# Optimization experiments

Hardware: AMD Instinct MI355X
Metric: run time of the kernel (lower is better)

Reference implementation:

```python
import jax, jax.numpy as jnp
import numpy as np

NUM_HEADS = 16
D_MODEL = 1024
DEPTH = D_MODEL // NUM_HEADS
B, S = 4, 1024  # q,k seq len = S; v seq len = S-1


def setup_inputs() -> dict:
    key = jax.random.key(0)
    ks = jax.random.split(key, 6)
    scale = 1.0 / np.sqrt(D_MODEL)
    return {
        "v": jax.random.normal(ks[0], (B, S - 1, D_MODEL), dtype=jnp.float32),
        "k": jax.random.normal(ks[1], (B, S, D_MODEL), dtype=jnp.float32),
        "q": jax.random.normal(ks[2], (B, S, D_MODEL), dtype=jnp.float32),
        "mask": jnp.zeros((B, S - 1, S - 1), dtype=jnp.float32),
        "Wv": jax.random.normal(ks[3], (D_MODEL, D_MODEL), dtype=jnp.float32) * scale,
        "bv": jnp.zeros((D_MODEL,), dtype=jnp.float32),
        "Wd": jax.random.normal(ks[4], (D_MODEL, D_MODEL), dtype=jnp.float32) * scale,
        "bd": jnp.zeros((D_MODEL,), dtype=jnp.float32),
    }


def _split_heads(x):
    # (B, T, d_model) -> (B, H, T, depth)
    b, t, _ = x.shape
    return x.reshape(b, t, NUM_HEADS, DEPTH).transpose(0, 2, 1, 3)


def reference(v, k, q, mask, Wv, bv, Wd, bd):
    # 3-D q/k path: qq=q, kk=k (q_layers/k_layers/wq/wk unused)
    vv = v @ Wv + bv                       # (B, S-1, d_model)
    qh = _split_heads(q)                   # (B, H, S, depth)
    kh = _split_heads(k)                   # (B, H, S, depth)
    vh = _split_heads(vv)                  # (B, H, S-1, depth)

    scores = jnp.einsum('bhqd,bhkd->bhqk', qh, kh)      # (B, H, S, S)
    scores = scores[:, :, 1:, :-1]                      # (B, H, S-1, S-1)
    dk = jnp.asarray(DEPTH, scores.dtype)
    nl = jax.nn.relu(scores / jnp.sqrt(dk))
    nl = nl + mask[:, None, :, :] * (-1e9)
    att = jax.nn.softmax(nl, axis=-1)                   # (B, H, S-1, S-1)

    out = jnp.einsum('bhqk,bhkd->bhqd', att, vh)        # (B, H, S-1, depth)
    out = out.transpose(0, 2, 1, 3).reshape(v.shape[0], -1, D_MODEL)  # (B, S-1, d_model)
    output = out @ Wd + bd
    return output, att
```

## Files before the change

### kernel.cpp

```cpp
#include <hip/hip_runtime.h>
#include <hip/hip_bf16.h>

#define NUM_HEADS 16
#define DM 1024
#define DEPTH 64
#define BB 4
#define SS 1024
#define SL 1023
#define M_ROWS (BB*SL)

typedef __attribute__((ext_vector_type(8))) short short8;
typedef __attribute__((ext_vector_type(4))) float floatx4;

__device__ inline unsigned short f2bf(float f) {
  __hip_bfloat16 hb = __float2bfloat16(f);
  return *reinterpret_cast<unsigned short*>(&hb);
}
__device__ inline short8 ld_frag(const unsigned short* p) {
  return *reinterpret_cast<const short8*>(p);
}

#define GLDS(g, l) __builtin_amdgcn_global_load_lds( \
    (const __attribute__((address_space(1))) void*)(g), \
    (__attribute__((address_space(3))) void*)(l), 16, 0, 0)

__global__ __launch_bounds__(256) void f32_to_bf16_vec(
    const float* __restrict__ in, unsigned short* __restrict__ out, int n8)
{
  int i = blockIdx.x * 256 + threadIdx.x;
  if (i >= n8) return;
  const float4 f0 = ((const float4*)in)[(size_t)i * 2];
  const float4 f1 = ((const float4*)in)[(size_t)i * 2 + 1];
  unsigned short t[8];
  t[0]=f2bf(f0.x); t[1]=f2bf(f0.y); t[2]=f2bf(f0.z); t[3]=f2bf(f0.w);
  t[4]=f2bf(f1.x); t[5]=f2bf(f1.y); t[6]=f2bf(f1.z); t[7]=f2bf(f1.w);
  ((uint4*)out)[i] = *(uint4*)t;
}

__global__ __launch_bounds__(256) void transpose_to_bf16(
    const float* __restrict__ W, unsigned short* __restrict__ WT)
{
  __shared__ unsigned short tile[64][72];
  const int tid = threadIdx.x;
  const int k0 = blockIdx.y * 64, n0 = blockIdx.x * 64;
  {
    const int kl = tid >> 2, nc = (tid & 3) * 16;
    const float* src = W + (size_t)(k0 + kl) * DM + n0 + nc;
    #pragma unroll
    for (int j = 0; j < 16; j += 4) {
      float4 f = *(const float4*)(src + j);
      tile[nc + j + 0][kl] = f2bf(f.x);
      tile[nc + j + 1][kl] = f2bf(f.y);
      tile[nc + j + 2][kl] = f2bf(f.z);
      tile[nc + j + 3][kl] = f2bf(f.w);
    }
  }
  __syncthreads();
  {
    const int nl = tid >> 2, kc = (tid & 3) * 16;
    unsigned short tmp[16];
    #pragma unroll
    for (int j = 0; j < 16; j++) tmp[j] = tile[nl][kc + j];
    unsigned short* dst = WT + (size_t)(n0 + nl) * DM + k0 + kc;
    *(uint4*)&dst[0] = *(uint4*)&tmp[0];
    *(uint4*)&dst[8] = *(uint4*)&tmp[8];
  }
}

template <bool OUT_BF16>
__global__ __launch_bounds__(256) void gemm_bt(
    const unsigned short* __restrict__ A,
    const unsigned short* __restrict__ BT,
    const float* __restrict__ bias,
    void* __restrict__ Cv, int M)
{
  constexpr int BM = 64, BN = 128, BK = 32;
  __shared__ __align__(16) unsigned short As[2][BM * BK];
  __shared__ __align__(16) unsigned short Bs[2][BN * BK];

  const int tid = threadIdx.x;
  const int w = tid >> 6, lane = tid & 63, q4 = lane >> 4, l16 = lane & 15;
  const int wm = w >> 1, wn = w & 1;
  const int rb = blockIdx.y * BM;
  const int cb = blockIdx.x * BN;

  const int a_row = tid >> 2;
  const int a_slot = (tid & 3) ^ ((a_row >> 1) & 3);
  int a_grow = rb + a_row; if (a_grow >= M) a_grow = M - 1;
  const unsigned short* a_src = A + (size_t)a_grow * DM + a_slot * 8;
  const int b_row0 = tid >> 2;
  const int b_row1 = 64 + (tid >> 2);
  const int b_slot0 = (tid & 3) ^ ((b_row0 >> 1) & 3);
  const int b_slot1 = (tid & 3) ^ ((b_row1 >> 1) & 3);
  const unsigned short* b_src0 = BT + (size_t)(cb + b_row0) * DM + b_slot0 * 8;
  const unsigned short* b_src1 = BT + (size_t)(cb + b_row1) * DM + b_slot1 * 8;

  int aoff[2], boff[4];
  #pragma unroll
  for (int i = 0; i < 2; i++) {
    int r = wm * 32 + i * 16 + l16;
    aoff[i] = r * BK + ((q4 ^ ((r >> 1) & 3)) * 8);
  }
  #pragma unroll
  for (int j = 0; j < 4; j++) {
    int r = wn * 64 + j * 16 + l16;
    boff[j] = r * BK + ((q4 ^ ((r >> 1) & 3)) * 8);
  }

  floatx4 acc[2][4];
  #pragma unroll
  for (int i = 0; i < 2; i++)
    #pragma unroll
    for (int j = 0; j < 4; j++) acc[i][j] = (floatx4){0.f,0.f,0.f,0.f};

  GLDS(a_src,  &As[0][tid * 8]);
  GLDS(b_src0, &Bs[0][tid * 8]);
  GLDS(b_src1, &Bs[0][2048 + tid * 8]);
  __syncthreads();

  int cur = 0;
  constexpr int NT = DM / BK;
  for (int t = 0; t < NT; ++t) {
    if (t + 1 < NT) {
      const int kn = (t + 1) * BK;
      GLDS(a_src + kn,  &As[cur ^ 1][tid * 8]);
      GLDS(b_src0 + kn, &Bs[cur ^ 1][tid * 8]);
      GLDS(b_src1 + kn, &Bs[cur ^ 1][2048 + tid * 8]);
    }
    short8 af[2], bfr[4];
    #pragma unroll
    for (int i = 0; i < 2; i++) af[i] = ld_frag(&As[cur][aoff[i]]);
    #pragma unroll
    for (int j = 0; j < 4; j++) bfr[j] = ld_frag(&Bs[cur][boff[j]]);
    #pragma unroll
    for (int i = 0; i < 2; i++)
      #pragma unroll
      for (int j = 0; j < 4; j++)
        acc[i][j] = __builtin_amdgcn_mfma_f32_16x16x32_bf16(af[i], bfr[j], acc[i][j], 0, 0, 0);
    __syncthreads();
    cur ^= 1;
  }

  #pragma unroll
  for (int j = 0; j < 4; j++) {
    int col = cb + wn * 64 + j * 16 + l16;
    float bb = bias[col];
    #pragma unroll
    for (int i = 0; i < 2; i++) {
      #pragma unroll
      for (int r = 0; r < 4; r++) {
        int m = rb + wm * 32 + i * 16 + q4 * 4 + r;
        if (m < M) {
          float val = acc[i][j][r] + bb;
          if (OUT_BF16) ((unsigned short*)Cv)[(size_t)m * DM + col] = f2bf(val);
          else          ((float*)Cv)[(size_t)m * DM + col] = val;
        }
      }
    }
  }
}

__global__ __launch_bounds__(256) void attn_kernel(
    const float* __restrict__ Q, const float* __restrict__ Kg,
    const float* __restrict__ Mask, const unsigned short* __restrict__ VV,
    float* __restrict__ Att, unsigned short* __restrict__ Out2)
{
  const int qt = blockIdx.x, h = blockIdx.y, b = blockIdx.z;
  const int tid = threadIdx.x;
  const int w = tid >> 6, lane = tid & 63, q4 = lane >> 4, l16 = lane & 15;
  const int qi0 = qt * 64;
  const int qb = w * 16;

  __shared__ unsigned short qsh[64][72];
  __shared__ unsigned short ksh[64][72];
  __shared__ unsigned short vshT[64][72];
  __shared__ unsigned short psh[4][16][72];

  {
    int qr = tid >> 2, d0 = (tid & 3) * 16;
    int qi = qi0 + qr;
    unsigned short tmp[16];
    if (qi < SL) {
      const float* src = Q + ((size_t)b * SS + qi + 1) * DM + h * DEPTH + d0;
      #pragma unroll
      for (int j = 0; j < 16; j += 4) {
        float4 f = *(const float4*)(src + j);
        tmp[j+0]=f2bf(f.x); tmp[j+1]=f2bf(f.y); tmp[j+2]=f2bf(f.z); tmp[j+3]=f2bf(f.w);
      }
    } else {
      #pragma unroll
      for (int j = 0; j < 16; j++) tmp[j] = 0;
    }
    *(uint4*)&qsh[qr][d0]     = *(uint4*)&tmp[0];
    *(uint4*)&qsh[qr][d0 + 8] = *(uint4*)&tmp[8];
  }

  auto stageK = [&](int kt) {
    int kr = tid >> 2, d0 = (tid & 3) * 16;
    int kj = kt * 64 + kr;
    unsigned short tmp[16];
    if (kj < SL) {
      const float* src = Kg + ((size_t)b * SS + kj) * DM + h * DEPTH + d0;
      #pragma unroll
      for (int j = 0; j < 16; j += 4) {
        float4 f = *(const float4*)(src + j);
        tmp[j+0]=f2bf(f.x); tmp[j+1]=f2bf(f.y); tmp[j+2]=f2bf(f.z); tmp[j+3]=f2bf(f.w);
      }
    } else {
      #pragma unroll
      for (int j = 0; j < 16; j++) tmp[j] = 0;
    }
    *(uint4*)&ksh[kr][d0]     = *(uint4*)&tmp[0];
    *(uint4*)&ksh[kr][d0 + 8] = *(uint4*)&tmp[8];
  };

  auto stageV = [&](int kt) {
    int d = tid & 63, k16 = (tid >> 6) * 16;
    unsigned short tmp[16];
    #pragma unroll
    for (int j = 0; j < 16; j++) {
      int kj = kt * 64 + k16 + j;
      tmp[j] = (kj < SL) ? VV[((size_t)b * SL + kj) * DM + h * DEPTH + d] : (unsigned short)0;
    }
    *(uint4*)&vshT[d][k16]     = *(uint4*)&tmp[0];
    *(uint4*)&vshT[d][k16 + 8] = *(uint4*)&tmp[8];
  };

  __syncthreads();

  float rsv[4] = {0.f, 0.f, 0.f, 0.f};
  for (int kt = 0; kt < 16; kt++) {
    __syncthreads();
    stageK(kt);
    __syncthreads();
    #pragma unroll
    for (int nt = 0; nt < 4; nt++) {
      floatx4 s = (floatx4){0.f,0.f,0.f,0.f};
      s = __builtin_amdgcn_mfma_f32_16x16x32_bf16(
            ld_frag(&qsh[qb + l16][q4*8]), ld_frag(&ksh[nt*16 + l16][q4*8]), s, 0,0,0);
      s = __builtin_amdgcn_mfma_f32_16x16x32_bf16(
            ld_frag(&qsh[qb + l16][32 + q4*8]), ld_frag(&ksh[nt*16 + l16][32 + q4*8]), s, 0,0,0);
      int kj = kt * 64 + nt * 16 + l16;
      bool kv = kj < SL;
      int qi_b = qi0 + qb + q4 * 4;
      const float* mp = Mask + ((size_t)b * SL + qi_b) * SL + kj;
      #pragma unroll
      for (int r = 0; r < 4; r++) {
        int qi = qi_b + r;
        float mval = (kv && qi < SL) ? mp[(size_t)r * SL] : 0.f;
        float sv = fmaxf(s[r] * 0.125f, 0.f) + mval * (-1e9f);
        float p = kv ? __expf(sv) : 0.f;
        rsv[r] += p;
      }
    }
  }
  #pragma unroll
  for (int r = 0; r < 4; r++) {
    #pragma unroll
    for (int off = 1; off < 16; off <<= 1) rsv[r] += __shfl_xor(rsv[r], off, 64);
  }
  float inv[4];
  #pragma unroll
  for (int r = 0; r < 4; r++) inv[r] = 1.f / rsv[r];

  floatx4 oacc[4];
  #pragma unroll
  for (int i = 0; i < 4; i++) oacc[i] = (floatx4){0.f,0.f,0.f,0.f};

  for (int kt = 0; kt < 16; kt++) {
    __syncthreads();
    stageK(kt);
    stageV(kt);
    __syncthreads();
    #pragma unroll
    for (int nt = 0; nt < 4; nt++) {
      floatx4 s = (floatx4){0.f,0.f,0.f,0.f};
      s = __builtin_amdgcn_mfma_f32_16x16x32_bf16(
            ld_frag(&qsh[qb + l16][q4*8]), ld_frag(&ksh[nt*16 + l16][q4*8]), s, 0,0,0);
      s = __builtin_amdgcn_mfma_f32_16x16x32_bf16(
            ld_frag(&qsh[qb + l16][32 + q4*8]), ld_frag(&ksh[nt*16 + l16][32 + q4*8]), s, 0,0,0);
      int kj = kt * 64 + nt * 16 + l16;
      bool kv = kj < SL;
      int qi_b = qi0 + qb + q4 * 4;
      const float* mp = Mask + ((size_t)b * SL + qi_b) * SL + kj;
      #pragma unroll
      for (int r = 0; r < 4; r++) {
        int qi = qi_b + r;
        bool qv = qi < SL;
        float mval = (kv && qv) ? mp[(size_t)r * SL] : 0.f;
        float sv = fmaxf(s[r] * 0.125f, 0.f) + mval * (-1e9f);
        float p = kv ? __expf(sv) : 0.f;
        float pn = p * inv[r];
        if (kv && qv)
          Att[(((size_t)(b * NUM_HEADS + h)) * SL + qi) * SL + kj] = pn;
        psh[w][q4 * 4 + r][nt * 16 + l16] = f2bf(pn);
      }
    }
    short8 pa0 = ld_frag(&psh[w][l16][q4 * 8]);
    short8 pa1 = ld_frag(&psh[w][l16][32 + q4 * 8]);
    #pragma unroll
    for (int nt2 = 0; nt2 < 4; nt2++) {
      oacc[nt2] = __builtin_amdgcn_mfma_f32_16x16x32_bf16(
                    pa0, ld_frag(&vshT[nt2*16 + l16][q4*8]), oacc[nt2], 0,0,0);
      oacc[nt2] = __builtin_amdgcn_mfma_f32_16x16x32_bf16(
                    pa1, ld_frag(&vshT[nt2*16 + l16][32 + q4*8]), oacc[nt2], 0,0,0);
    }
  }

  #pragma unroll
  for (int nt2 = 0; nt2 < 4; nt2++) {
    #pragma unroll
    for (int r = 0; r < 4; r++) {
      int qi = qi0 + qb + q4 * 4 + r;
      if (qi < SL)
        Out2[((size_t)b * SL + qi) * DM + h * DEPTH + nt2 * 16 + l16] = f2bf(oacc[nt2][r]);
    }
  }
}

extern "C" void kernel_launch(void* const* d_in, const int* in_sizes, int n_in,
                              void* d_out, int out_size, void* d_ws, size_t ws_size,
                              hipStream_t stream) {
  const float* v    = (const float*)d_in[0];
  const float* k    = (const float*)d_in[1];
  const float* q    = (const float*)d_in[2];
  const float* mask = (const float*)d_in[3];
  const float* Wv   = (const float*)d_in[4];
  const float* bv   = (const float*)d_in[5];
  const float* Wd   = (const float*)d_in[6];
  const float* bd   = (const float*)d_in[7];

  float* out = (float*)d_out;
  float* att = out + (size_t)M_ROWS * DM;
  unsigned short* vv   = (unsigned short*)d_ws;
  unsigned short* out2 = vv + (size_t)M_ROWS * DM;

  unsigned short* WvT = (unsigned short*)att;
  unsigned short* vbf = WvT + (size_t)DM * DM;
  unsigned short* WdT = vv;

  const int n8 = (M_ROWS * DM) / 8;

  f32_to_bf16_vec<<<dim3((n8 + 255) / 256), 256, 0, stream>>>(v, vbf, n8);
  transpose_to_bf16<<<dim3(16, 16), 256, 0, stream>>>(Wv, WvT);
  gemm_bt<true><<<dim3(DM/128, (M_ROWS+63)/64), 256, 0, stream>>>(vbf, WvT, bv, (void*)vv, M_ROWS);
  attn_kernel<<<dim3(16, NUM_HEADS, BB), 256, 0, stream>>>(q, k, mask, vv, att, out2);
  transpose_to_bf16<<<dim3(16, 16), 256, 0, stream>>>(Wd, WdT);
  gemm_bt<false><<<dim3(DM/128, (M_ROWS+63)/64), 256, 0, stream>>>(out2, WdT, bd, (void*)out, M_ROWS);
}
```

Before: 667.0 us.

## Triple-buffer GEMM with BK=64 and swap attention grid order

The bf16 GEMM now uses a K tile of 64 with a three-stage LDS ring, fed by direct global-to-LDS loads. It uses explicit vmcnt waits and barriers so two future tiles stay in flight while the current one runs through MFMA, with a new XOR swizzle over 8 groups. The fp32 output GEMM uses nontemporal stores. The attention grid is reordered so heads vary fastest, which changes L2 locality between neighbouring blocks. The larger LDS footprint may reduce occupancy, and the hand-written waitcnt counts must match the number of issued loads exactly.

```diff
diff --git a/kernel.cpp b/kernel.cpp
--- a/kernel.cpp
+++ b/kernel.cpp
@@ -19,6 +19,8 @@
 __device__ inline short8 ld_frag(const unsigned short* p) {
   return *reinterpret_cast<const short8*>(p);
 }
+
+#define SWZ(row, g) (((g) ^ ((row) & 7)))
 
 #define GLDS(g, l) __builtin_amdgcn_global_load_lds( \
     (const __attribute__((address_space(1))) void*)(g), \
@@ -74,9 +76,9 @@
     const float* __restrict__ bias,
     void* __restrict__ Cv, int M)
 {
-  constexpr int BM = 64, BN = 128, BK = 32;
-  __shared__ __align__(16) unsigned short As[2][BM * BK];
-  __shared__ __align__(16) unsigned short Bs[2][BN * BK];
+  constexpr int BM = 64, BN = 128, BK = 64;
+  __shared__ __align__(16) unsigned short As[3][BM * BK];
+  __shared__ __align__(16) unsigned short Bs[3][BN * BK];
 
   const int tid = threadIdx.x;
   const int w = tid >> 6, lane = tid & 63, q4 = lane >> 4, l16 = lane & 15;
@@ -84,28 +86,44 @@
   const int rb = blockIdx.y * BM;
   const int cb = blockIdx.x * BN;
 
-  const int a_row = tid >> 2;
-  const int a_slot = (tid & 3) ^ ((a_row >> 1) & 3);
-  int a_grow = rb + a_row; if (a_grow >= M) a_grow = M - 1;
-  const unsigned short* a_src = A + (size_t)a_grow * DM + a_slot * 8;
-  const int b_row0 = tid >> 2;
-  const int b_row1 = 64 + (tid >> 2);
-  const int b_slot0 = (tid & 3) ^ ((b_row0 >> 1) & 3);
-  const int b_slot1 = (tid & 3) ^ ((b_row1 >> 1) & 3);
-  const unsigned short* b_src0 = BT + (size_t)(cb + b_row0) * DM + b_slot0 * 8;
-  const unsigned short* b_src1 = BT + (size_t)(cb + b_row1) * DM + b_slot1 * 8;
-
-  int aoff[2], boff[4];
-  #pragma unroll
-  for (int i = 0; i < 2; i++) {
-    int r = wm * 32 + i * 16 + l16;
-    aoff[i] = r * BK + ((q4 ^ ((r >> 1) & 3)) * 8);
-  }
-  #pragma unroll
-  for (int j = 0; j < 4; j++) {
-    int r = wn * 64 + j * 16 + l16;
-    boff[j] = r * BK + ((q4 ^ ((r >> 1) & 3)) * 8);
-  }
+  const int wbase = __builtin_amdgcn_readfirstlane(w * 512);
+
+  const int srow = tid >> 3;
+  const int lg   = (tid & 7) ^ (srow & 7);
+  int ar0 = rb + srow;       if (ar0 >= M) ar0 = M - 1;
+  int ar1 = rb + 32 + srow;  if (ar1 >= M) ar1 = M - 1;
+  const unsigned short* a_src0 = A + (size_t)ar0 * DM + lg * 8;
+  const unsigned short* a_src1 = A + (size_t)ar1 * DM + lg * 8;
+  const unsigned short* b_src0 = BT + (size_t)(cb      + srow) * DM + lg * 8;
+  const unsigned short* b_src1 = BT + (size_t)(cb + 32 + srow) * DM + lg * 8;
+  const unsigned short* b_src2 = BT + (size_t)(cb + 64 + srow) * DM + lg * 8;
+  const unsigned short* b_src3 = BT + (size_t)(cb + 96 + srow) * DM + lg * 8;
+
+  auto stage = [&](int t, unsigned short* Ab, unsigned short* Bb) {
+    const int kn = t * BK;
+    GLDS(a_src0 + kn, Ab + wbase);
+    GLDS(a_src1 + kn, Ab + 2048 + wbase);
+    GLDS(b_src0 + kn, Bb + wbase);
+    GLDS(b_src1 + kn, Bb + 2048 + wbase);
+    GLDS(b_src2 + kn, Bb + 4096 + wbase);
+    GLDS(b_src3 + kn, Bb + 6144 + wbase);
+  };
+
+  int aoff[2][2], boff[4][2];
+  #pragma unroll
+  for (int i = 0; i < 2; i++)
+    #pragma unroll
+    for (int hf = 0; hf < 2; hf++) {
+      int r = wm * 32 + i * 16 + l16;
+      aoff[i][hf] = r * BK + SWZ(r, q4 + 4 * hf) * 8;
+    }
+  #pragma unroll
+  for (int j = 0; j < 4; j++)
+    #pragma unroll
+    for (int hf = 0; hf < 2; hf++) {
+      int r = wn * 64 + j * 16 + l16;
+      boff[j][hf] = r * BK + SWZ(r, q4 + 4 * hf) * 8;
+    }
 
   floatx4 acc[2][4];
   #pragma unroll
@@ -113,32 +131,51 @@
     #pragma unroll
     for (int j = 0; j < 4; j++) acc[i][j] = (floatx4){0.f,0.f,0.f,0.f};
 
-  GLDS(a_src,  &As[0][tid * 8]);
-  GLDS(b_src0, &Bs[0][tid * 8]);
-  GLDS(b_src1, &Bs[0][2048 + tid * 8]);
-  __syncthreads();
+  stage(0, As[0], Bs[0]);
+  stage(1, As[1], Bs[1]);
+  stage(2, As[2], Bs[2]);
 
   int cur = 0;
   constexpr int NT = DM / BK;
   for (int t = 0; t < NT; ++t) {
-    if (t + 1 < NT) {
-      const int kn = (t + 1) * BK;
-      GLDS(a_src + kn,  &As[cur ^ 1][tid * 8]);
-      GLDS(b_src0 + kn, &Bs[cur ^ 1][tid * 8]);
-      GLDS(b_src1 + kn, &Bs[cur ^ 1][2048 + tid * 8]);
-    }
-    short8 af[2], bfr[4];
-    #pragma unroll
-    for (int i = 0; i < 2; i++) af[i] = ld_frag(&As[cur][aoff[i]]);
-    #pragma unroll
-    for (int j = 0; j < 4; j++) bfr[j] = ld_frag(&Bs[cur][boff[j]]);
-    #pragma unroll
-    for (int i = 0; i < 2; i++)
-      #pragma unroll
-      for (int j = 0; j < 4; j++)
-        acc[i][j] = __builtin_amdgcn_mfma_f32_16x16x32_bf16(af[i], bfr[j], acc[i][j], 0, 0, 0);
-    __syncthreads();
-    cur ^= 1;
+    if (t < NT - 2)       asm volatile("s_waitcnt vmcnt(12)" ::: "memory");
+    else if (t == NT - 2) asm volatile("s_waitcnt vmcnt(6)"  ::: "memory");
+    else                  asm volatile("s_waitcnt vmcnt(0)"  ::: "memory");
+    __builtin_amdgcn_sched_barrier(0);
+    __builtin_amdgcn_s_barrier();
+    __builtin_amdgcn_sched_barrier(0);
+
+    unsigned short* Ab = As[cur];
+    unsigned short* Bb = Bs[cur];
+    short8 af[2][2], bfr[4][2];
+    #pragma unroll
+    for (int hf = 0; hf < 2; hf++) {
+      af[0][hf] = ld_frag(Ab + aoff[0][hf]);
+      af[1][hf] = ld_frag(Ab + aoff[1][hf]);
+      bfr[0][hf] = ld_frag(Bb + boff[0][hf]);
+      bfr[1][hf] = ld_frag(Bb + boff[1][hf]);
+      bfr[2][hf] = ld_frag(Bb + boff[2][hf]);
+      bfr[3][hf] = ld_frag(Bb + boff[3][hf]);
+    }
+    asm volatile("s_waitcnt lgkmcnt(0)" ::: "memory");
+    __builtin_amdgcn_sched_barrier(0);
+    __builtin_amdgcn_s_barrier();
+    __builtin_amdgcn_sched_barrier(0);
+
+    if (t + 3 < NT) stage(t + 3, Ab, Bb);
+
+    #pragma unroll
+    for (int hf = 0; hf < 2; hf++) {
+      acc[0][0] = __builtin_amdgcn_mfma_f32_16x16x32_bf16(af[0][hf], bfr[0][hf], acc[0][0], 0,0,0);
+      acc[0][1] = __builtin_amdgcn_mfma_f32_16x16x32_bf16(af[0][hf], bfr[1][hf], acc[0][1], 0,0,0);
+      acc[0][2] = __builtin_amdgcn_mfma_f32_16x16x32_bf16(af[0][hf], bfr[2][hf], acc[0][2], 0,0,0);
+      acc[0][3] = __builtin_amdgcn_mfma_f32_16x16x32_bf16(af[0][hf], bfr[3][hf], acc[0][3], 0,0,0);
+      acc[1][0] = __builtin_amdgcn_mfma_f32_16x16x32_bf16(af[1][hf], bfr[0][hf], acc[1][0], 0,0,0);
+      acc[1][1] = __builtin_amdgcn_mfma_f32_16x16x32_bf16(af[1][hf], bfr[1][hf], acc[1][1], 0,0,0);
+      acc[1][2] = __builtin_amdgcn_mfma_f32_16x16x32_bf16(af[1][hf], bfr[2][hf], acc[1][2], 0,0,0);
+      acc[1][3] = __builtin_amdgcn_mfma_f32_16x16x32_bf16(af[1][hf], bfr[3][hf], acc[1][3], 0,0,0);
+    }
+    cur = (cur == 2) ? 0 : cur + 1;
   }
 
   #pragma unroll
@@ -153,7 +190,7 @@
         if (m < M) {
           float val = acc[i][j][r] + bb;
           if (OUT_BF16) ((unsigned short*)Cv)[(size_t)m * DM + col] = f2bf(val);
-          else          ((float*)Cv)[(size_t)m * DM + col] = val;
+          else __builtin_nontemporal_store(val, &((float*)Cv)[(size_t)m * DM + col]);
         }
       }
     }
@@ -165,7 +202,7 @@
     const float* __restrict__ Mask, const unsigned short* __restrict__ VV,
     float* __restrict__ Att, unsigned short* __restrict__ Out2)
 {
-  const int qt = blockIdx.x, h = blockIdx.y, b = blockIdx.z;
+  const int h = blockIdx.x, qt = blockIdx.y, b = blockIdx.z;
   const int tid = threadIdx.x;
   const int w = tid >> 6, lane = tid & 63, q4 = lane >> 4, l16 = lane & 15;
   const int qi0 = qt * 64;
@@ -344,7 +381,7 @@
   f32_to_bf16_vec<<<dim3((n8 + 255) / 256), 256, 0, stream>>>(v, vbf, n8);
   transpose_to_bf16<<<dim3(16, 16), 256, 0, stream>>>(Wv, WvT);
   gemm_bt<true><<<dim3(DM/128, (M_ROWS+63)/64), 256, 0, stream>>>(vbf, WvT, bv, (void*)vv, M_ROWS);
-  attn_kernel<<<dim3(16, NUM_HEADS, BB), 256, 0, stream>>>(q, k, mask, vv, att, out2);
+  attn_kernel<<<dim3(NUM_HEADS, 16, BB), 256, 0, stream>>>(q, k, mask, vv, att, out2);
   transpose_to_bf16<<<dim3(16, 16), 256, 0, stream>>>(Wd, WdT);
   gemm_bt<false><<<dim3(DM/128, (M_ROWS+63)/64), 256, 0, stream>>>(out2, WdT, bd, (void*)out, M_ROWS);
 }
```

After: 643.5 us. 1.04x faster.
